# Performance work log

Measured on AMD Instinct MI355X. Metric: run time of the kernel, lower is better.

Reference implementation:

```python
import jax, jax.numpy as jnp
import numpy as np

B, T, D, H = 4, 2048, 1024, 16
HD = D // H  # head_dim = 64


def setup_inputs() -> dict:
    key = jax.random.key(0)
    k1, k2, k3 = jax.random.split(key, 3)
    x = jax.random.normal(k1, (B, T, D), dtype=jnp.float32)
    # rotary cache: (T, head_dim/2, 2) holding (cos, sin)
    inv_freq = 1.0 / (10000.0 ** (jnp.arange(0, HD, 2, dtype=jnp.float32) / HD))  # (HD/2,)
    t = jnp.arange(T, dtype=jnp.float32)
    freqs = jnp.einsum('t,f->tf', t, inv_freq)  # (T, HD/2)
    rope = jnp.stack([jnp.cos(freqs), jnp.sin(freqs)], axis=-1)  # (T, HD/2, 2)
    # causal boolean attn mask, broadcastable (1,1,T,T)
    mask = jnp.tril(jnp.ones((T, T), dtype=bool))[None, None]
    # params (bias-free linears), scaled like nn.Linear default init
    W_attn = jax.random.normal(k2, (3 * D, D), dtype=jnp.float32) / np.sqrt(D)
    W_proj = jax.random.normal(k3, (D, D), dtype=jnp.float32) / np.sqrt(D)
    return {"x": x, "rope": rope, "mask": mask, "W_attn": W_attn, "W_proj": W_proj}


def apply_rope(x, rope):
    # x: (B, T, H, HD); rope: (T, HD/2, 2)
    b, t, h, hd = x.shape
    xr = x.reshape(b, t, h, hd // 2, 2)
    x1, x2 = xr[..., 0], xr[..., 1]
    cos = rope[None, :, None, :, 0]  # (1, T, 1, HD/2)
    sin = rope[None, :, None, :, 1]
    out = jnp.stack([x1 * cos - x2 * sin, x1 * sin + x2 * cos], axis=-1)
    return out.reshape(b, t, h, hd)


def reference(x, rope, mask, W_attn, W_proj):
    b, t, d = x.shape
    qkv = jnp.einsum('btd,ed->bte', x, W_attn)  # (B, T, 3D)
    q, k, v = jnp.split(qkv, 3, axis=2)
    q = apply_rope(q.reshape(b, t, H, HD), rope)
    k = apply_rope(k.reshape(b, t, H, HD), rope)
    v = v.reshape(b, t, H, HD)
    # (B, H, T, HD)
    q = q.transpose(0, 2, 1, 3)
    k = k.transpose(0, 2, 1, 3)
    v = v.transpose(0, 2, 1, 3)
    scale = 1.0 / np.sqrt(HD)
    scores = jnp.einsum('bhqd,bhkd->bhqk', q, k) * scale
    scores = jnp.where(mask, scores, jnp.finfo(scores.dtype).min)
    attn = jax.nn.softmax(scores, axis=-1)
    o = jnp.einsum('bhqk,bhkd->bhqd', attn, v)
    o = o.transpose(0, 2, 1, 3).reshape(b, t, d)
    return jnp.einsum('btd,ed->bte', o, W_proj)
```

## Files before the change

### kernel.cpp

```cpp
#include <hip/hip_runtime.h>

typedef unsigned short u16;
typedef unsigned int u32;
typedef unsigned long long u64;
typedef __bf16 v8bf __attribute__((ext_vector_type(8)));
typedef __bf16 v4bf __attribute__((ext_vector_type(4)));
typedef float v4f __attribute__((ext_vector_type(4)));
typedef float v16f __attribute__((ext_vector_type(16)));
typedef u32 v4u __attribute__((ext_vector_type(4)));

#define BB 4
#define TT 2048
#define HH 16
#define DD 1024

__device__ __forceinline__ u16 f2bf(float f){
  u32 u = __float_as_uint(f);
  u32 r = u + 0x7FFFu + ((u >> 16) & 1u);
  return (u16)(r >> 16);
}
__device__ __forceinline__ float bf2f(u16 h){ return __uint_as_float(((u32)h) << 16); }
__device__ __forceinline__ v16f z16(){
  v16f z;
#pragma unroll
  for (int i = 0; i < 16; i++) z[i] = 0.f;
  return z;
}
__device__ __forceinline__ u32 cvtpk(float lo, float hi){
  u32 d;
  asm("v_cvt_pk_bf16_f32 %0, %1, %2" : "=v"(d) : "v"(lo), "v"(hi));
  return d;
}
__device__ __forceinline__ void swap32(u32 &a, u32 &b){
  asm volatile("v_permlane32_swap_b32 %0, %1" : "+v"(a), "+v"(b));
}

typedef __attribute__((address_space(1))) const void gas_t;
typedef __attribute__((address_space(3))) void las_t;
__device__ __forceinline__ void gl_lds16(const void* g, void* l){
  __builtin_amdgcn_global_load_lds((gas_t*)g, (las_t*)l, 16, 0, 0);
}

__global__ __launch_bounds__(256) void k_convert(
    const float* __restrict__ x, const float* __restrict__ wa,
    const float* __restrict__ wp, u16* __restrict__ xb,
    u16* __restrict__ wab, u16* __restrict__ wpb){
  int i = blockIdx.x * 256 + threadIdx.x;
  const int nxq = (BB*TT*DD) / 4;
  const int naq = (3*DD*DD) / 4;
  const float* src; u16* dst; int j;
  if (i < nxq)            { src = x;  dst = xb;  j = i; }
  else if (i < nxq + naq) { src = wa; dst = wab; j = i - nxq; }
  else                    { src = wp; dst = wpb; j = i - nxq - naq; }
  float4 v = reinterpret_cast<const float4*>(src)[j];
  u64 p = (u64)f2bf(v.x) | ((u64)f2bf(v.y) << 16)
        | ((u64)f2bf(v.z) << 32) | ((u64)f2bf(v.w) << 48);
  reinterpret_cast<u64*>(dst)[j] = p;
}

__global__ __launch_bounds__(256) void k_gemm_bt(
    const u16* __restrict__ A, const u16* __restrict__ Bt,
    const float* __restrict__ rope,
    int M, int N, int K, int mode, float* __restrict__ Cf,
    u16* __restrict__ qo, u16* __restrict__ ko, u16* __restrict__ vo){
  __shared__ char smem[32768];
  char* As = smem;
  char* Bs = smem + 16384;
  const int t = threadIdx.x;
  const int lane = t & 63, w = t >> 6;
  const int c = lane & 15, g = lane >> 4;
  const int nbn = N >> 7;
  const int chunk = gridDim.x >> 3;
  const int swzb = (blockIdx.x & 7) * chunk + (blockIdx.x >> 3);
  const int bm = swzb / nbn, bn = swzb % nbn;
  const long arow0 = (long)bm * 128;
  const long brow0 = (long)bn * 128;
  const int wrow = (w >> 1) * 64, wcol = (w & 1) * 64;

  v4f acc[4][4];
#pragma unroll
  for (int i = 0; i < 4; i++)
#pragma unroll
    for (int j = 0; j < 4; j++){ v4f z = {0.f,0.f,0.f,0.f}; acc[i][j] = z; }

  for (int k0 = 0; k0 < K; k0 += 64){
    __syncthreads();
#pragma unroll
    for (int i = 0; i < 4; i++){
      int slot = t + i * 256;
      int row  = slot >> 3;
      int cb   = (slot & 7) << 4;
      int scb  = cb ^ ((row & 7) << 4);
      gl_lds16((const char*)A  + ((arow0 + row) * (long)K + k0) * 2 + scb,
               As + ((t & 192) + i * 256) * 16);
      gl_lds16((const char*)Bt + ((brow0 + row) * (long)K + k0) * 2 + scb,
               Bs + ((t & 192) + i * 256) * 16);
    }
    __syncthreads();

    v8bf af[4][2], bfr[4][2];
#pragma unroll
    for (int mt = 0; mt < 4; mt++){
      int row = wrow + mt * 16 + c;
      int sw  = (row & 7) << 4;
#pragma unroll
      for (int ks = 0; ks < 2; ks++)
        af[mt][ks] = *(const v8bf*)(As + row * 128 + ((ks * 64 + g * 16) ^ sw));
    }
#pragma unroll
    for (int nt = 0; nt < 4; nt++){
      int row = wcol + nt * 16 + c;
      int sw  = (row & 7) << 4;
#pragma unroll
      for (int ks = 0; ks < 2; ks++)
        bfr[nt][ks] = *(const v8bf*)(Bs + row * 128 + ((ks * 64 + g * 16) ^ sw));
    }
#pragma unroll
    for (int mt = 0; mt < 4; mt++)
#pragma unroll
      for (int nt = 0; nt < 4; nt++)
#pragma unroll
        for (int ks = 0; ks < 2; ks++)
          acc[mt][nt] = __builtin_amdgcn_mfma_f32_16x16x32_bf16(
              af[mt][ks], bfr[nt][ks], acc[mt][nt], 0, 0, 0);
  }

  if (mode == 1){
#pragma unroll
    for (int mt = 0; mt < 4; mt++)
#pragma unroll
      for (int nt = 0; nt < 4; nt++)
#pragma unroll
        for (int r = 0; r < 4; r++){
          long row = arow0 + wrow + mt * 16 + g * 4 + r;
          long col = brow0 + wcol + nt * 16 + c;
          Cf[row * N + col] = acc[mt][nt][r];
        }
  } else {
    const int t0 = (int)(arow0 & 2047);
    __syncthreads();
#pragma unroll
    for (int l = 0; l < 8; l++)
      gl_lds16((const char*)rope + (size_t)t0 * 256 + (size_t)(t + l * 256) * 16,
               smem + ((t & 192) + l * 256) * 16);
    __syncthreads();

    const long bb = arow0 >> 11;
#pragma unroll
    for (int mt = 0; mt < 4; mt++){
      const int tposb = wrow + mt * 16 + g * 4;
#pragma unroll
      for (int nt = 0; nt < 4; nt++){
        int e    = (int)brow0 + wcol + nt * 16 + c;
        int tsel = e >> 10;
        int hh   = (e >> 6) & 15;
        int d    = e & 63;
        if (tsel == 2){
          v4bf pk;
#pragma unroll
          for (int r = 0; r < 4; r++) pk[r] = (__bf16)acc[mt][nt][r];
          *(v4bf*)(vo + (((bb * HH + hh) * 64 + d) << 11) + t0 + tposb) = pk;
        } else {
          const float qs = tsel ? 1.0f : 0.18033688011112042f;
          const int f = d >> 1;
          const bool odd = d & 1;
          u16* dst = tsel ? ko : qo;
          long base = ((bb * HH + hh) * TT + t0 + tposb) * 64 + d;
#pragma unroll
          for (int r = 0; r < 4; r++){
            float v = acc[mt][nt][r];
            float2 cn = *(const float2*)(smem + (tposb + r) * 256 + f * 8);
            float px = __shfl_xor(v, 1, 64);
            float o = odd ? (px * cn.y + v * cn.x) : (v * cn.x - px * cn.y);
            dst[base + (long)r * 64] = f2bf(o * qs);
          }
        }
      }
    }
  }
}

__global__ __launch_bounds__(256) void k_attn(
    const u16* __restrict__ Q, const u16* __restrict__ K,
    const u16* __restrict__ Vt, u16* __restrict__ O){
  __shared__ char smem[16384];
  char* ksm = smem;
  char* vsm = smem + 8192;
  int bx = blockIdx.x;
  int bh = bx & 63;
  int bt = 15 - (bx >> 6);
  int q0 = bt * 128;
  int b = bh >> 4, h = bh & 15;
  const u16* Qb = Q  + (size_t)bh * TT * 64;
  const u16* Kb = K  + (size_t)bh * TT * 64;
  const u16* Vb = Vt + (size_t)bh * 64 * TT;
  const int t = threadIdx.x, lane = t & 63, w = t >> 6;
  const int c = lane & 31, hi = lane >> 5;
  const int swz = (c & 7) << 4;
  const int wq0 = q0 + w * 32;

  v8bf qf[4];
  {
    const u16* qrow = Qb + (size_t)(wq0 + c) * 64 + hi * 8;
#pragma unroll
    for (int kc = 0; kc < 4; kc++) qf[kc] = *(const v8bf*)(qrow + kc * 16);
  }

  float l_ = 0.f;
  v16f accO0 = z16(), accO1 = z16();

  for (int kv0 = 0; kv0 < q0 + 128; kv0 += 64){
    __syncthreads();
#pragma unroll
    for (int i = 0; i < 2; i++){
      int s   = t + i * 256;
      int row = s >> 3;
      int cb  = (s & 7) << 4;
      int scb = cb ^ ((row & 7) << 4);
      gl_lds16((const char*)Kb + (size_t)(kv0 + row) * 128 + scb,
               ksm + ((t & 192) + i * 256) * 16);
      gl_lds16((const char*)Vb + (size_t)row * (TT * 2) + (size_t)kv0 * 2 + scb,
               vsm + ((t & 192) + i * 256) * 16);
    }
    __syncthreads();

    if (kv0 <= wq0 + 31){
      v16f s0 = z16(), s1 = z16();
      __builtin_amdgcn_s_setprio(1);
#pragma unroll
      for (int kc = 0; kc < 4; kc++){
        int off = (kc * 32 + hi * 16) ^ swz;
        v8bf a0 = *(const v8bf*)(ksm + c * 128 + off);
        v8bf a1 = *(const v8bf*)(ksm + (32 + c) * 128 + off);
        s0 = __builtin_amdgcn_mfma_f32_32x32x16_bf16(a0, qf[kc], s0, 0, 0, 0);
        s1 = __builtin_amdgcn_mfma_f32_32x32x16_bf16(a1, qf[kc], s1, 0, 0, 0);
      }
      __builtin_amdgcn_s_setprio(0);
      if (kv0 + 63 > wq0){
        int q = wq0 + c;
#pragma unroll
        for (int r = 0; r < 16; r++){
          int crow = (r & 3) + 8 * (r >> 2) + 4 * hi;
          if (kv0 + crow > q)      s0[r] = -1e30f;
          if (kv0 + 32 + crow > q) s1[r] = -1e30f;
        }
      }
      float sum = 0.f;
#pragma unroll
      for (int r = 0; r < 16; r++){
        float p0 = __builtin_amdgcn_exp2f(s0[r] - 12.0f);
        float p1 = __builtin_amdgcn_exp2f(s1[r] - 12.0f);
        s0[r] = p0; s1[r] = p1;
        sum += p0 + p1;
      }
      sum += __shfl_xor(sum, 32, 64);
      l_ += sum;
      v8bf pbf[4];
      {
        u32 wd[16];
#pragma unroll
        for (int i = 0; i < 8; i++) wd[i]     = cvtpk(s0[2*i], s0[2*i+1]);
#pragma unroll
        for (int i = 0; i < 8; i++) wd[8 + i] = cvtpk(s1[2*i], s1[2*i+1]);
        swap32(wd[0], wd[2]);  swap32(wd[1], wd[3]);
        swap32(wd[4], wd[6]);  swap32(wd[5], wd[7]);
        swap32(wd[8], wd[10]); swap32(wd[9], wd[11]);
        swap32(wd[12], wd[14]); swap32(wd[13], wd[15]);
        v4u u0 = {wd[0], wd[1], wd[2], wd[3]};
        v4u u1 = {wd[4], wd[5], wd[6], wd[7]};
        v4u u2 = {wd[8], wd[9], wd[10], wd[11]};
        v4u u3 = {wd[12], wd[13], wd[14], wd[15]};
        pbf[0] = __builtin_bit_cast(v8bf, u0);
        pbf[1] = __builtin_bit_cast(v8bf, u1);
        pbf[2] = __builtin_bit_cast(v8bf, u2);
        pbf[3] = __builtin_bit_cast(v8bf, u3);
      }
      __builtin_amdgcn_s_setprio(1);
#pragma unroll
      for (int kc = 0; kc < 4; kc++){
        int off = (kc * 32 + hi * 16) ^ swz;
        v8bf va0 = *(const v8bf*)(vsm + c * 128 + off);
        v8bf va1 = *(const v8bf*)(vsm + (32 + c) * 128 + off);
        accO0 = __builtin_amdgcn_mfma_f32_32x32x16_bf16(va0, pbf[kc], accO0, 0, 0, 0);
        accO1 = __builtin_amdgcn_mfma_f32_32x32x16_bf16(va1, pbf[kc], accO1, 0, 0, 0);
      }
      __builtin_amdgcn_s_setprio(0);
    }
  }

  float inv = __builtin_amdgcn_rcpf(l_);
  int q = wq0 + c;
  u16* orow = O + ((size_t)(b * TT + q)) * DD + h * 64;
#pragma unroll
  for (int q4 = 0; q4 < 4; q4++){
    v4bf o0, o1;
#pragma unroll
    for (int j = 0; j < 4; j++){
      o0[j] = (__bf16)(accO0[q4 * 4 + j] * inv);
      o1[j] = (__bf16)(accO1[q4 * 4 + j] * inv);
    }
    *(v4bf*)(orow + q4 * 8 + hi * 4)      = o0;
    *(v4bf*)(orow + 32 + q4 * 8 + hi * 4) = o1;
  }
}

extern "C" void kernel_launch(void* const* d_in, const int* in_sizes, int n_in,
                              void* d_out, int out_size, void* d_ws, size_t ws_size,
                              hipStream_t stream){
  const float* x    = (const float*)d_in[0];
  const float* rope = (const float*)d_in[1];
  const float* Wa   = (const float*)d_in[3];
  const float* Wp   = (const float*)d_in[4];

  char* ws = (char*)d_ws;
  u16* xb  = (u16*)(ws);
  u16* wab = (u16*)(ws + (16u << 20));
  u16* wpb = (u16*)(ws + (22u << 20));
  u16* qb  = (u16*)(ws + (24u << 20));
  u16* kb  = (u16*)(ws + (40u << 20));
  u16* vtb = (u16*)(ws + (56u << 20));
  u16* ob  = xb;

  k_convert<<<dim3(12288), dim3(256), 0, stream>>>(x, Wa, Wp, xb, wab, wpb);
  k_gemm_bt<<<dim3(24 * 64), dim3(256), 0, stream>>>(
      xb, wab, rope, 8192, 3072, 1024, 0, nullptr, qb, kb, vtb);
  k_attn<<<dim3(1024), dim3(256), 0, stream>>>(qb, kb, vtb, ob);
  k_gemm_bt<<<dim3(8 * 64), dim3(256), 0, stream>>>(
      ob, wpb, nullptr, 8192, 1024, 1024, 1, (float*)d_out,
      nullptr, nullptr, nullptr);
}
```

Measured before the change: 164.9 us.

## Double attention query tile per block to reuse K/V loads across two subtiles

Each attention block now covers 256 query rows, with each wave handling two 32-row subtiles, so every K/V tile staged in shared memory feeds twice as many MFMAs. The grid is halved to 512 blocks and the block-to-tile mapping is reordered to pair heavy and light causal tiles across scheduling waves. This cuts global-to-LDS traffic and barrier count per unit of work. In exchange it doubles accumulator register use, which may lower occupancy, and leaves fewer blocks for load balancing.

```diff
diff --git a/kernel.cpp b/kernel.cpp
--- a/kernel.cpp
+++ b/kernel.cpp
@@ -188,8 +188,9 @@
   char* vsm = smem + 8192;
   int bx = blockIdx.x;
   int bh = bx & 63;
-  int bt = 15 - (bx >> 6);
-  int q0 = bt * 128;
+  int bt4 = (bx >> 6) & 3;
+  int bt = (bx >> 8) ? bt4 : 7 - bt4;
+  int q0 = bt * 256;
   int b = bh >> 4, h = bh & 15;
   const u16* Qb = Q  + (size_t)bh * TT * 64;
   const u16* Kb = K  + (size_t)bh * TT * 64;
@@ -197,19 +198,22 @@
   const int t = threadIdx.x, lane = t & 63, w = t >> 6;
   const int c = lane & 31, hi = lane >> 5;
   const int swz = (c & 7) << 4;
-  const int wq0 = q0 + w * 32;
-
-  v8bf qf[4];
-  {
-    const u16* qrow = Qb + (size_t)(wq0 + c) * 64 + hi * 8;
-#pragma unroll
-    for (int kc = 0; kc < 4; kc++) qf[kc] = *(const v8bf*)(qrow + kc * 16);
-  }
-
-  float l_ = 0.f;
-  v16f accO0 = z16(), accO1 = z16();
-
-  for (int kv0 = 0; kv0 < q0 + 128; kv0 += 64){
+  const int wq0 = q0 + w * 64;
+
+  v8bf qf[2][4];
+#pragma unroll
+  for (int qi = 0; qi < 2; qi++){
+    const u16* qrow = Qb + (size_t)(wq0 + qi * 32 + c) * 64 + hi * 8;
+#pragma unroll
+    for (int kc = 0; kc < 4; kc++) qf[qi][kc] = *(const v8bf*)(qrow + kc * 16);
+  }
+
+  float l_[2] = {0.f, 0.f};
+  v16f acc[2][2];
+#pragma unroll
+  for (int qi = 0; qi < 2; qi++){ acc[qi][0] = z16(); acc[qi][1] = z16(); }
+
+  for (int kv0 = 0; kv0 < q0 + 256; kv0 += 64){
     __syncthreads();
 #pragma unroll
     for (int i = 0; i < 2; i++){
@@ -224,7 +228,10 @@
     }
     __syncthreads();
 
-    if (kv0 <= wq0 + 31){
+#pragma unroll
+    for (int qi = 0; qi < 2; qi++){
+      const int mq0 = wq0 + qi * 32;
+      if (kv0 > mq0 + 31) continue;
       v16f s0 = z16(), s1 = z16();
       __builtin_amdgcn_s_setprio(1);
 #pragma unroll
@@ -232,12 +239,12 @@
         int off = (kc * 32 + hi * 16) ^ swz;
         v8bf a0 = *(const v8bf*)(ksm + c * 128 + off);
         v8bf a1 = *(const v8bf*)(ksm + (32 + c) * 128 + off);
-        s0 = __builtin_amdgcn_mfma_f32_32x32x16_bf16(a0, qf[kc], s0, 0, 0, 0);
-        s1 = __builtin_amdgcn_mfma_f32_32x32x16_bf16(a1, qf[kc], s1, 0, 0, 0);
+        s0 = __builtin_amdgcn_mfma_f32_32x32x16_bf16(a0, qf[qi][kc], s0, 0, 0, 0);
+        s1 = __builtin_amdgcn_mfma_f32_32x32x16_bf16(a1, qf[qi][kc], s1, 0, 0, 0);
       }
       __builtin_amdgcn_s_setprio(0);
-      if (kv0 + 63 > wq0){
-        int q = wq0 + c;
+      if (kv0 + 63 > mq0){
+        int q = mq0 + c;
 #pragma unroll
         for (int r = 0; r < 16; r++){
           int crow = (r & 3) + 8 * (r >> 2) + 4 * hi;
@@ -254,7 +261,7 @@
         sum += p0 + p1;
       }
       sum += __shfl_xor(sum, 32, 64);
-      l_ += sum;
+      l_[qi] += sum;
       v8bf pbf[4];
       {
         u32 wd[16];
@@ -281,26 +288,29 @@
         int off = (kc * 32 + hi * 16) ^ swz;
         v8bf va0 = *(const v8bf*)(vsm + c * 128 + off);
         v8bf va1 = *(const v8bf*)(vsm + (32 + c) * 128 + off);
-        accO0 = __builtin_amdgcn_mfma_f32_32x32x16_bf16(va0, pbf[kc], accO0, 0, 0, 0);
-        accO1 = __builtin_amdgcn_mfma_f32_32x32x16_bf16(va1, pbf[kc], accO1, 0, 0, 0);
+        acc[qi][0] = __builtin_amdgcn_mfma_f32_32x32x16_bf16(va0, pbf[kc], acc[qi][0], 0, 0, 0);
+        acc[qi][1] = __builtin_amdgcn_mfma_f32_32x32x16_bf16(va1, pbf[kc], acc[qi][1], 0, 0, 0);
       }
       __builtin_amdgcn_s_setprio(0);
     }
   }
 
-  float inv = __builtin_amdgcn_rcpf(l_);
-  int q = wq0 + c;
-  u16* orow = O + ((size_t)(b * TT + q)) * DD + h * 64;
-#pragma unroll
-  for (int q4 = 0; q4 < 4; q4++){
-    v4bf o0, o1;
-#pragma unroll
-    for (int j = 0; j < 4; j++){
-      o0[j] = (__bf16)(accO0[q4 * 4 + j] * inv);
-      o1[j] = (__bf16)(accO1[q4 * 4 + j] * inv);
-    }
-    *(v4bf*)(orow + q4 * 8 + hi * 4)      = o0;
-    *(v4bf*)(orow + 32 + q4 * 8 + hi * 4) = o1;
+#pragma unroll
+  for (int qi = 0; qi < 2; qi++){
+    float inv = __builtin_amdgcn_rcpf(l_[qi]);
+    int q = wq0 + qi * 32 + c;
+    u16* orow = O + ((size_t)(b * TT + q)) * DD + h * 64;
+#pragma unroll
+    for (int q4 = 0; q4 < 4; q4++){
+      v4bf o0, o1;
+#pragma unroll
+      for (int j = 0; j < 4; j++){
+        o0[j] = (__bf16)(acc[qi][0][q4 * 4 + j] * inv);
+        o1[j] = (__bf16)(acc[qi][1][q4 * 4 + j] * inv);
+      }
+      *(v4bf*)(orow + q4 * 8 + hi * 4)      = o0;
+      *(v4bf*)(orow + 32 + q4 * 8 + hi * 4) = o1;
+    }
   }
 }
 
@@ -324,7 +334,7 @@
   k_convert<<<dim3(12288), dim3(256), 0, stream>>>(x, Wa, Wp, xb, wab, wpb);
   k_gemm_bt<<<dim3(24 * 64), dim3(256), 0, stream>>>(
       xb, wab, rope, 8192, 3072, 1024, 0, nullptr, qb, kb, vtb);
-  k_attn<<<dim3(1024), dim3(256), 0, stream>>>(qb, kb, vtb, ob);
+  k_attn<<<dim3(512), dim3(256), 0, stream>>>(qb, kb, vtb, ob);
   k_gemm_bt<<<dim3(8 * 64), dim3(256), 0, stream>>>(
       ob, wpb, nullptr, 8192, 1024, 1024, 1, (float*)d_out,
       nullptr, nullptr, nullptr);
```

Result: slower. 184.4 us (+11.8%).
